# Optimization experiments

Measured on AMD Instinct MI355X. Metric: run time of the kernel, lower is better.

Reference implementation:

```python
import jax, jax.numpy as jnp
import numpy as np

# Regular batched tree: BS roots, arity A, depth D (root=level 0, leaves=level D)
BS, A, D = 32, 4, 6
V, E, H = 50000, 256, 256
LEVEL_SIZES = [BS * A ** d for d in range(D + 1)]
OFFSETS = np.concatenate([[0], np.cumsum(LEVEL_SIZES)]).astype(np.int64)
TOTAL = int(OFFSETS[-1])  # 174752


def gru_cell(x, h, w_ih, w_hh, b_ih, b_hh):
    # torch nn.GRU single step, gate order (r, z, n)
    gi = x @ w_ih.T + b_ih
    gh = h @ w_hh.T + b_hh
    ir, iz, inn = jnp.split(gi, 3, axis=-1)
    hr, hz, hn = jnp.split(gh, 3, axis=-1)
    r = jax.nn.sigmoid(ir + hr)
    z = jax.nn.sigmoid(iz + hz)
    n = jnp.tanh(inn + r * hn)
    return (1.0 - z) * n + z * h


def child_attention(h_last, sent_weight, sent_bias, context_weight):
    # Reproduces hidden_per_child stacking: ch[g,c,i,:] = h_last[g,c] if c==i else 0.
    G, S, _ = h_last.shape
    eye = jnp.eye(S, dtype=h_last.dtype)
    ch = h_last[:, :, None, :] * eye[None, :, :, None]          # [G,S(c),S(i),H]
    t1 = jnp.tanh(jnp.einsum('gcih,hk->gcik', ch, sent_weight) + sent_bias[0])
    u = jnp.tanh(jnp.einsum('gcik,ko->gci', t1, context_weight))  # [G,S,S]
    w = jax.nn.softmax(u, axis=1)                                # softmax over c (the P axis)
    return jnp.einsum('gci,gcih->gih', w, ch)                    # [G,S,H]


def setup_inputs() -> dict:
    key = jax.random.key(0)
    ks = jax.random.split(key, 9)
    s = 1.0 / np.sqrt(H)
    return {
        'tokens': jax.random.randint(ks[0], (TOTAL,), 0, V, dtype=jnp.int32),
        'embedding': jax.random.normal(ks[1], (V, E), jnp.float32) * 0.1,
        'w_ih': jax.random.uniform(ks[2], (3 * H, E), jnp.float32, -s, s),
        'w_hh': jax.random.uniform(ks[3], (3 * H, H), jnp.float32, -s, s),
        'b_ih': jax.random.uniform(ks[4], (3 * H,), jnp.float32, -s, s),
        'b_hh': jax.random.uniform(ks[5], (3 * H,), jnp.float32, -s, s),
        'sent_weight': jax.random.normal(ks[6], (H, H), jnp.float32) * 0.05,
        'sent_bias': jax.random.normal(ks[7], (1, H), jnp.float32) * 0.05,
        'context_weight': jax.random.normal(ks[8], (H, 1), jnp.float32) * 0.05,
    }


def reference(tokens, embedding, w_ih, w_hh, b_ih, b_hh, sent_weight, sent_bias, context_weight):
    def tok(d):
        return tokens[int(OFFSETS[d]):int(OFFSETS[d + 1])]

    gru = lambda x, h: gru_cell(x, h, w_ih, w_hh, b_ih, b_hh)

    # leaves: no children -> zero initial hidden
    h_levels = {D: gru(embedding[tok(D)], jnp.zeros((LEVEL_SIZES[D], H), jnp.float32))}

    for d in range(D - 1, -1, -1):
        h_child = h_levels[d + 1].reshape(-1, A, H)   # [N_d, A, H]
        # duplicate index_copy in torch: only last child's hidden survives per parent
        h_last = h_child[:, A - 1, :]                 # [N_d, H]
        S = BS if d == 0 else A                       # call size: bs at root, A siblings otherwise
        groups = h_last.reshape(-1, S, H)
        chs = child_attention(groups, sent_weight, sent_bias, context_weight).reshape(-1, H)
        h_levels[d] = gru(embedding[tok(d)], chs)

    # final max over node_list: root entry has all bs rows; every other call's entry has
    # only row b = hn of the LAST sibling (duplicate valid_indices), zeros elsewhere.
    out = jnp.maximum(jnp.zeros((BS, H), jnp.float32), h_levels[0])
    for d in range(1, D + 1):
        last_sib = h_levels[d].reshape(BS, -1, A, H)[:, :, A - 1, :].max(axis=1)
        out = jnp.maximum(out, last_sib)
    return out
```

## Files before the change

kernel.cpp:

```cpp
#include <hip/hip_runtime.h>
#include <hip/hip_bf16.h>
#include <math.h>


typedef unsigned short u16;
typedef unsigned int u32;
typedef __attribute__((ext_vector_type(8))) short s8;
typedef __attribute__((ext_vector_type(4))) float f4;
#define MFMA16(a, b, c) __builtin_amdgcn_mfma_f32_16x16x32_bf16(a, b, c, 0, 0, 0)

__device__ __forceinline__ u16 f2bf(float f) {
  u32 x = __float_as_uint(f);
  return (u16)((x + 0x7fffu + ((x >> 16) & 1u)) >> 16);
}
__device__ __forceinline__ float bf2f(u16 u) { return __uint_as_float(((u32)u) << 16); }
__device__ __forceinline__ float sigmoidf_(float x) {
  return __builtin_amdgcn_rcpf(1.f + __builtin_amdgcn_exp2f(-1.4426950408889634f * x));
}
__device__ __forceinline__ float tanhf_(float x) {
  x = fminf(fmaxf(x, -15.f), 15.f);
  float t = __builtin_amdgcn_exp2f(-2.8853900817779268f * x);
  return 1.f - 2.f * t * __builtin_amdgcn_rcpf(1.f + t);
}
__device__ __forceinline__ void gload_lds16(const void* g, void* l) {
  typedef const __attribute__((address_space(1))) unsigned int* gp_t;
  typedef __attribute__((address_space(3))) unsigned int* lp_t;
  __builtin_amdgcn_global_load_lds((gp_t)g, (lp_t)l, 16, 0, 0);
}
__device__ __forceinline__ void stage_row(const float* __restrict__ emb, int tok,
                                          u16* aX, int r, int lane) {
  float4 v = ((const float4*)(emb + (size_t)tok * 256))[lane];
  uint2 val = {(u32)f2bf(v.x) | ((u32)f2bf(v.y) << 16),
               (u32)f2bf(v.z) | ((u32)f2bf(v.w) << 16)};
  *(uint2*)&aX[r * 256 + ((((lane >> 1)) ^ (r & 7)) << 3) + (lane & 1) * 4] = val;
}

__global__ void prep_pack(const float* __restrict__ wih, const float* __restrict__ whh,
                          const float* __restrict__ sw, const float* __restrict__ sb,
                          const float* __restrict__ cw,
                          u16* __restrict__ wihP, u16* __restrict__ whhPh,
                          u16* __restrict__ whhPl, u16* __restrict__ swPh,
                          float* __restrict__ u0p, int* __restrict__ outI) {
  int b = blockIdx.x, t = threadIdx.x;
  if (b == 320) {
    #pragma unroll
    for (int k = 0; k < 32; ++k) outI[k * 256 + t] = 0;
    if (t < 64) {
      float s = 0.f;
      #pragma unroll
      for (int q = 0; q < 4; ++q) { int k = t + 64 * q; s += tanhf(sb[k]) * cw[k]; }
      #pragma unroll
      for (int off = 32; off >= 1; off >>= 1) s += __shfl_xor(s, off);
      if (t == 0) u0p[0] = tanhf(s);
    }
    return;
  }
  int g = b * 256 + t;
  const float* src;
  u16* dst;
  int idx, NF, lomode, trans;
  if (g < 24576)      { idx = g;         src = wih; dst = wihP;  NF = 48; lomode = 0; trans = 1; }
  else if (g < 49152) { idx = g - 24576; src = whh; dst = whhPh; NF = 48; lomode = 0; trans = 1; }
  else if (g < 73728) { idx = g - 49152; src = whh; dst = whhPl; NF = 48; lomode = 1; trans = 1; }
  else                { idx = g - 73728; src = sw;  dst = swPh;  NF = 16; lomode = 0; trans = 0; }
  int lane = idx & 63;
  int t2 = idx >> 6;
  int nf = t2 % NF, kb = t2 / NF;
  int n = nf * 16 + (lane & 15);
  int k0 = kb * 32 + (lane >> 4) * 8;
  float v[8];
  if (trans) {
    const float4* p = (const float4*)(src + (size_t)n * 256 + k0);
    float4 a = p[0], b2 = p[1];
    v[0] = a.x; v[1] = a.y; v[2] = a.z; v[3] = a.w;
    v[4] = b2.x; v[5] = b2.y; v[6] = b2.z; v[7] = b2.w;
  } else {
    #pragma unroll
    for (int j = 0; j < 8; ++j) v[j] = src[(size_t)(k0 + j) * 256 + n];
  }
  u16 o[8];
  #pragma unroll
  for (int j = 0; j < 8; ++j) {
    u16 hi = f2bf(v[j]);
    o[j] = lomode ? f2bf(v[j] - bf2f(hi)) : hi;
  }
  u32* d = (u32*)(dst + (size_t)idx * 8);
  #pragma unroll
  for (int j = 0; j < 4; ++j) d[j] = (u32)o[2 * j] | ((u32)o[2 * j + 1] << 16);
}

__global__ __launch_bounds__(512, 2)
void levelAB_kernel(const int* __restrict__ t6, const int* __restrict__ t5,
                    const float* __restrict__ emb,
                    const u16* __restrict__ wihP, const u16* __restrict__ whhPh,
                    const u16* __restrict__ whhPl, const u16* __restrict__ swPh,
                    const float* __restrict__ bih, const float* __restrict__ bhh,
                    const float* __restrict__ sb, const float* __restrict__ cw,
                    const float* __restrict__ u0p,
                    u16* __restrict__ Hs5Hi, u16* __restrict__ Hs5Lo,
                    int* __restrict__ outI) {
  __shared__ u16 aX6[32768];
  __shared__ u16 aX5[8192];
  __shared__ u16 aH[2][8192];
  __shared__ float pm[8][32];
  __shared__ float scl[32];

  const int t = threadIdx.x;
  const int rb = blockIdx.x;
  const int lane = t & 63, w = t >> 6;
  const int asub = lane >> 4, l15 = lane & 15;
  const float LN3 = 1.0986122886681098f;

  {
    #pragma unroll
    for (int rr = 0; rr < 16; ++rr) {
      int r = 16 * w + rr;
      int tok = t6[4 * (128 * rb + r) + 3];
      stage_row(emb, tok, aX6, r, lane);
    }
    #pragma unroll
    for (int rr = 0; rr < 4; ++rr) {
      int r = 4 * w + rr;
      int tok = t5[4 * (32 * rb + r) + 3];
      stage_row(emb, tok, aX5, r, lane);
    }
  }
  __syncthreads();

  #pragma unroll 1
  for (int pass = 0; pass < 4; ++pass) {
    const int sp = pass >> 1, jc = pass & 1;
    const int cfx = 2 * w + jc;
    f4 gi[3][4];
    #pragma unroll
    for (int g = 0; g < 3; ++g)
      #pragma unroll
      for (int mf = 0; mf < 4; ++mf) gi[g][mf] = (f4){0.f, 0.f, 0.f, 0.f};
    s8 bw[2][3];
    auto LB = [&](int kb, int pb) {
      #pragma unroll
      for (int g = 0; g < 3; ++g)
        bw[pb][g] = *(const s8*)&wihP[((size_t)(kb * 48 + 16 * g + cfx) * 64 + lane) * 8];
    };
    LB(0, 0);
    #pragma unroll
    for (int kb = 0; kb < 8; ++kb) {
      const int pb = kb & 1;
      if (kb < 7) LB(kb + 1, pb ^ 1);
      s8 axh[4];
      #pragma unroll
      for (int mf = 0; mf < 4; ++mf) {
        int abase = (64 * sp + 16 * mf + l15) * 256 + (((kb * 4 + asub) ^ (l15 & 7)) << 3);
        axh[mf] = *(const s8*)&aX6[abase];
      }
      #pragma unroll
      for (int g = 0; g < 3; ++g)
        #pragma unroll
        for (int mf = 0; mf < 4; ++mf)
          gi[g][mf] = MFMA16(axh[mf], bw[pb][g], gi[g][mf]);
    }
    const int col = 16 * cfx + l15;
    const float bi0 = bih[col], bi1 = bih[256 + col], bi2 = bih[512 + col];
    const float bh0 = bhh[col], bh1 = bhh[256 + col], bh2 = bhh[512 + col];
    float cm = -1e30f;
    #pragma unroll
    for (int mf = 0; mf < 4; ++mf) {
      #pragma unroll
      for (int j = 0; j < 4; ++j) {
        float r = sigmoidf_(gi[0][mf][j] + bi0 + bh0);
        float z = sigmoidf_(gi[1][mf][j] + bi1 + bh1);
        float n = tanhf_(gi[2][mf][j] + bi2 + r * bh2);
        float h = (1.f - z) * n;
        if (j == 3) {
          int ci = 16 * sp + 4 * mf + asub;
          u16 hi = f2bf(h);
          u16 lo = f2bf(h - bf2f(hi));
          int hidx = ((col >> 3) * 32 + ci) * 8 + (col & 7);
          aH[0][hidx] = hi;
          aH[1][hidx] = lo;
        }
        cm = fmaxf(cm, h);
      }
    }
    cm = fmaxf(cm, __shfl_xor(cm, 16));
    cm = fmaxf(cm, __shfl_xor(cm, 32));
    if (asub == 0)
      atomicMax(outI + (size_t)(rb >> 3) * 256 + col, __float_as_int(cm));
  }
  __syncthreads();

  f4 sa[2][2];
  #pragma unroll
  for (int jc = 0; jc < 2; ++jc)
    #pragma unroll
    for (int mf = 0; mf < 2; ++mf) sa[jc][mf] = (f4){0.f, 0.f, 0.f, 0.f};
  {
    s8 bsw[2][2];
    auto LSW = [&](int kb, int pb) {
      #pragma unroll
      for (int jc = 0; jc < 2; ++jc)
        bsw[pb][jc] = *(const s8*)&swPh[((size_t)(kb * 16 + 2 * w + jc) * 64 + lane) * 8];
    };
    LSW(0, 0);
    #pragma unroll
    for (int kb = 0; kb < 8; ++kb) {
      const int pb = kb & 1;
      if (kb < 7) LSW(kb + 1, pb ^ 1);
      s8 ahh[2], ahl[2];
      #pragma unroll
      for (int mf = 0; mf < 2; ++mf) {
        int abase = ((kb * 4 + asub) * 32 + 16 * mf + l15) * 8;
        ahh[mf] = *(const s8*)&aH[0][abase];
        ahl[mf] = *(const s8*)&aH[1][abase];
      }
      #pragma unroll
      for (int jc = 0; jc < 2; ++jc) {
        sa[jc][0] = MFMA16(ahh[0], bsw[pb][jc], sa[jc][0]);
        sa[jc][1] = MFMA16(ahh[1], bsw[pb][jc], sa[jc][1]);
        sa[jc][0] = MFMA16(ahl[0], bsw[pb][jc], sa[jc][0]);
        sa[jc][1] = MFMA16(ahl[1], bsw[pb][jc], sa[jc][1]);
      }
    }
  }
  {
    float part[2][4] = {{0.f, 0.f, 0.f, 0.f}, {0.f, 0.f, 0.f, 0.f}};
    #pragma unroll
    for (int jc = 0; jc < 2; ++jc) {
      int k = 16 * (2 * w + jc) + l15;
      float sbk = sb[k], cwk = cw[k];
      #pragma unroll
      for (int mf = 0; mf < 2; ++mf)
        #pragma unroll
        for (int j = 0; j < 4; ++j) part[mf][j] += tanhf_(sa[jc][mf][j] + sbk) * cwk;
    }
    #pragma unroll
    for (int mf = 0; mf < 2; ++mf)
      #pragma unroll
      for (int j = 0; j < 4; ++j) {
        part[mf][j] += __shfl_xor(part[mf][j], 1);
        part[mf][j] += __shfl_xor(part[mf][j], 2);
        part[mf][j] += __shfl_xor(part[mf][j], 4);
        part[mf][j] += __shfl_xor(part[mf][j], 8);
      }
    if (l15 == 0) {
      #pragma unroll
      for (int mf = 0; mf < 2; ++mf)
        #pragma unroll
        for (int j = 0; j < 4; ++j) pm[w][16 * mf + 4 * asub + j] = part[mf][j];
    }
    __syncthreads();
    if (t < 32) {
      float v = 0.f;
      #pragma unroll
      for (int q = 0; q < 8; ++q) v += pm[q][t];
      scl[t] = sigmoidf_(tanhf_(v) - u0p[0] - LN3);
    }
    __syncthreads();
  }
  #pragma unroll 1
  for (int pass = 0; pass < 4; ++pass) {
    const int p = pass >> 1, mf = pass & 1;
    const int cf = w + 8 * p;
    f4 gi5[3], gh5[3];
    #pragma unroll
    for (int g = 0; g < 3; ++g) {
      gi5[g] = (f4){0.f, 0.f, 0.f, 0.f};
      gh5[g] = (f4){0.f, 0.f, 0.f, 0.f};
    }
    #pragma unroll
    for (int kb = 0; kb < 8; ++kb) {
      s8 bwi[3], bwh[3], bwl[3];
      #pragma unroll
      for (int g = 0; g < 3; ++g) {
        size_t bo = ((size_t)(kb * 48 + 16 * g + cf) * 64 + lane) * 8;
        bwi[g] = *(const s8*)&wihP[bo];
        bwh[g] = *(const s8*)&whhPh[bo];
        bwl[g] = *(const s8*)&whhPl[bo];
      }
      int axb = (16 * mf + l15) * 256 + (((kb * 4 + asub) ^ (l15 & 7)) << 3);
      s8 axh = *(const s8*)&aX5[axb];
      int abase = ((kb * 4 + asub) * 32 + 16 * mf + l15) * 8;
      s8 ahh = *(const s8*)&aH[0][abase];
      s8 ahl = *(const s8*)&aH[1][abase];
      #pragma unroll
      for (int g = 0; g < 3; ++g) {
        gi5[g] = MFMA16(axh, bwi[g], gi5[g]);
        gh5[g] = MFMA16(ahh, bwh[g], gh5[g]);
        gh5[g] = MFMA16(ahl, bwh[g], gh5[g]);
        gh5[g] = MFMA16(ahh, bwl[g], gh5[g]);
      }
    }
    const int col = 16 * cf + l15;
    const float bi0 = bih[col], bi1 = bih[256 + col], bi2 = bih[512 + col];
    const float bh0 = bhh[col], bh1 = bhh[256 + col], bh2 = bhh[512 + col];
    const int r0 = 16 * mf + 4 * asub;
    float cm = -1e30f;
    #pragma unroll
    for (int j = 0; j < 4; ++j) {
      const int row = r0 + j;
      const int i = 32 * rb + row;
      float sc = scl[row];
      float ir = gi5[0][j] + bi0;
      float iz = gi5[1][j] + bi1;
      float inn = gi5[2][j] + bi2;
      float g0 = bh0 + sc * gh5[0][j];
      float g1 = bh1 + sc * gh5[1][j];
      float g2 = bh2 + sc * gh5[2][j];
      int hidx = ((col >> 3) * 32 + row) * 8 + (col & 7);
      float hp = sc * (bf2f(aH[0][hidx]) + bf2f(aH[1][hidx]));
      float r = sigmoidf_(ir + g0);
      float z = sigmoidf_(iz + g1);
      float n = tanhf_(inn + r * g2);
      float h = (1.f - z) * n + z * hp;
      if (j == 3) {
        u16 hi = f2bf(h);
        u16 lo = f2bf(h - bf2f(hi));
        Hs5Hi[(size_t)(i >> 2) * 256 + col] = hi;
        Hs5Lo[(size_t)(i >> 2) * 256 + col] = lo;
      }
      cm = fmaxf(cm, h);
    }
    cm = fmaxf(cm, __shfl_xor(cm, 16));
    cm = fmaxf(cm, __shfl_xor(cm, 32));
    if (asub == 0)
      atomicMax(outI + (size_t)(rb >> 3) * 256 + col, __float_as_int(cm));
  }
}

__global__ __launch_bounds__(512, 2)
void levelB_kernel(const int* __restrict__ tokens, const float* __restrict__ emb,
                   const u16* __restrict__ wihP, const u16* __restrict__ whhPh,
                   const u16* __restrict__ whhPl, const u16* __restrict__ swPh,
                   const float* __restrict__ bih, const float* __restrict__ bhh,
                   const float* __restrict__ sb, const float* __restrict__ cw,
                   const float* __restrict__ u0p,
                   const u16* __restrict__ HpHi, const u16* __restrict__ HpLo,
                   u16* __restrict__ HoutHi, u16* __restrict__ HoutLo,
                   int* __restrict__ outI, float logSm1, int bshift) {
  __shared__ u16 aX[8192];
  __shared__ u16 aH[2][8192];
  __shared__ float pm[8][32];
  __shared__ float scl[32];

  const int t = threadIdx.x;
  const int rb = blockIdx.x >> 1, cb = blockIdx.x & 1;
  const int i0 = rb * 32;
  const int lane = t & 63, w = t >> 6;

  {
    int row = lane & 31;
    const u16* sh = HpHi + ((size_t)(i0 + row) << 8);
    const u16* sl = HpLo + ((size_t)(i0 + row) << 8);
    #pragma unroll
    for (int c = 0; c < 2; ++c) {
      int cg = w * 4 + c * 2 + (lane >> 5);
      int lb = w * 1024 + c * 512;
      gload_lds16(sh + (cg << 3), &aH[0][lb]);
      gload_lds16(sl + (cg << 3), &aH[1][lb]);
    }
  }
  {
    #pragma unroll
    for (int rr = 0; rr < 4; ++rr) {
      int r = 4 * w + rr;
      int tok = tokens[4 * (i0 + r) + 3];
      stage_row(emb, tok, aX, r, lane);
    }
  }
  __syncthreads();

  const int asub = lane >> 4, l15 = lane & 15;
  const int cfg = 8 * cb + w;

  f4 gi[3][2], gh[3][2], sa[2][2];
  #pragma unroll
  for (int g = 0; g < 3; ++g)
    #pragma unroll
    for (int mf = 0; mf < 2; ++mf) {
      gi[g][mf] = (f4){0.f, 0.f, 0.f, 0.f};
      gh[g][mf] = (f4){0.f, 0.f, 0.f, 0.f};
    }
  #pragma unroll
  for (int jc = 0; jc < 2; ++jc)
    #pragma unroll
    for (int mf = 0; mf < 2; ++mf) sa[jc][mf] = (f4){0.f, 0.f, 0.f, 0.f};

  #pragma unroll
  for (int kb = 0; kb < 8; ++kb) {
    s8 bwi[3], bwh[3], bwl[3], bsw[2];
    #pragma unroll
    for (int g = 0; g < 3; ++g) {
      size_t bo = ((size_t)(kb * 48 + 16 * g + cfg) * 64 + lane) * 8;
      bwi[g] = *(const s8*)&wihP[bo];
      bwh[g] = *(const s8*)&whhPh[bo];
      bwl[g] = *(const s8*)&whhPl[bo];
    }
    #pragma unroll
    for (int jc = 0; jc < 2; ++jc) {
      size_t so = ((size_t)(kb * 16 + 2 * w + jc) * 64 + lane) * 8;
      bsw[jc] = *(const s8*)&swPh[so];
    }
    s8 axh[2], ahh[2], ahl[2];
    #pragma unroll
    for (int mf = 0; mf < 2; ++mf) {
      int axb = (16 * mf + l15) * 256 + (((kb * 4 + asub) ^ (l15 & 7)) << 3);
      axh[mf] = *(const s8*)&aX[axb];
      int abase = ((kb * 4 + asub) * 32 + 16 * mf + l15) * 8;
      ahh[mf] = *(const s8*)&aH[0][abase];
      ahl[mf] = *(const s8*)&aH[1][abase];
    }
    #pragma unroll
    for (int g = 0; g < 3; ++g) {
      gi[g][0] = MFMA16(axh[0], bwi[g], gi[g][0]);
      gi[g][1] = MFMA16(axh[1], bwi[g], gi[g][1]);
      gh[g][0] = MFMA16(ahh[0], bwh[g], gh[g][0]);
      gh[g][1] = MFMA16(ahh[1], bwh[g], gh[g][1]);
      gh[g][0] = MFMA16(ahl[0], bwh[g], gh[g][0]);
      gh[g][1] = MFMA16(ahl[1], bwh[g], gh[g][1]);
      gh[g][0] = MFMA16(ahh[0], bwl[g], gh[g][0]);
      gh[g][1] = MFMA16(ahh[1], bwl[g], gh[g][1]);
    }
    #pragma unroll
    for (int jc = 0; jc < 2; ++jc) {
      sa[jc][0] = MFMA16(ahh[0], bsw[jc], sa[jc][0]);
      sa[jc][1] = MFMA16(ahh[1], bsw[jc], sa[jc][1]);
      sa[jc][0] = MFMA16(ahl[0], bsw[jc], sa[jc][0]);
      sa[jc][1] = MFMA16(ahl[1], bsw[jc], sa[jc][1]);
    }
  }

  {
    float part[2][4] = {{0.f, 0.f, 0.f, 0.f}, {0.f, 0.f, 0.f, 0.f}};
    #pragma unroll
    for (int jc = 0; jc < 2; ++jc) {
      int k = 16 * (2 * w + jc) + l15;
      float sbk = sb[k], cwk = cw[k];
      #pragma unroll
      for (int mf = 0; mf < 2; ++mf)
        #pragma unroll
        for (int j = 0; j < 4; ++j) part[mf][j] += tanhf_(sa[jc][mf][j] + sbk) * cwk;
    }
    #pragma unroll
    for (int mf = 0; mf < 2; ++mf)
      #pragma unroll
      for (int j = 0; j < 4; ++j) {
        part[mf][j] += __shfl_xor(part[mf][j], 1);
        part[mf][j] += __shfl_xor(part[mf][j], 2);
        part[mf][j] += __shfl_xor(part[mf][j], 4);
        part[mf][j] += __shfl_xor(part[mf][j], 8);
      }
    if (l15 == 0) {
      #pragma unroll
      for (int mf = 0; mf < 2; ++mf)
        #pragma unroll
        for (int j = 0; j < 4; ++j) pm[w][16 * mf + 4 * asub + j] = part[mf][j];
    }
    __syncthreads();
    if (t < 32) {
      float v = 0.f;
      #pragma unroll
      for (int q = 0; q < 8; ++q) v += pm[q][t];
      scl[t] = sigmoidf_(tanhf_(v) - u0p[0] - logSm1);
    }
    __syncthreads();
  }

  {
    const int col = 16 * cfg + l15;
    const float bi0 = bih[col], bi1 = bih[256 + col], bi2 = bih[512 + col];
    const float bh0 = bhh[col], bh1 = bhh[256 + col], bh2 = bhh[512 + col];
    float cmax = -1e30f;
    #pragma unroll
    for (int mf = 0; mf < 2; ++mf) {
      const int r0 = 16 * mf + 4 * asub;
      #pragma unroll
      for (int j = 0; j < 4; ++j) {
        const int row = r0 + j;
        const int i = i0 + row;
        float sc = scl[row];
        float ir = gi[0][mf][j] + bi0;
        float iz = gi[1][mf][j] + bi1;
        float inn = gi[2][mf][j] + bi2;
        float g0 = bh0 + sc * gh[0][mf][j];
        float g1 = bh1 + sc * gh[1][mf][j];
        float g2 = bh2 + sc * gh[2][mf][j];
        int hidx = ((col >> 3) * 32 + row) * 8 + (col & 7);
        float hp = sc * (bf2f(aH[0][hidx]) + bf2f(aH[1][hidx]));
        float r = sigmoidf_(ir + g0);
        float z = sigmoidf_(iz + g1);
        float n = tanhf_(inn + r * g2);
        float h = (1.f - z) * n + z * hp;
        if ((i & 3) == 3) {
          u16 hi = f2bf(h);
          u16 lo = f2bf(h - bf2f(hi));
          HoutHi[(size_t)(i >> 2) * 256 + col] = hi;
          HoutLo[(size_t)(i >> 2) * 256 + col] = lo;
        }
        cmax = fmaxf(cmax, h);
      }
    }
    cmax = fmaxf(cmax, __shfl_xor(cmax, 16));
    cmax = fmaxf(cmax, __shfl_xor(cmax, 32));
    if (asub == 0)
      atomicMax(outI + (size_t)(i0 >> bshift) * 256 + col, __float_as_int(cmax));
  }
}

struct Bregs {
  s8 wi[3], wh[3], wl[3], sw[4];
};
__device__ __forceinline__ void loadB(int kb, int cf, int wq, int lane,
                                      const u16* __restrict__ wihP,
                                      const u16* __restrict__ whhPh,
                                      const u16* __restrict__ whhPl,
                                      const u16* __restrict__ swPh, Bregs& r) {
  #pragma unroll
  for (int g = 0; g < 3; ++g) {
    size_t bo = ((size_t)(kb * 48 + 16 * g + cf) * 64 + lane) * 8;
    r.wi[g] = *(const s8*)&wihP[bo];
    r.wh[g] = *(const s8*)&whhPh[bo];
    r.wl[g] = *(const s8*)&whhPl[bo];
  }
  #pragma unroll
  for (int c = 0; c < 4; ++c) {
    size_t so = ((size_t)(kb * 16 + 4 * wq + c) * 64 + lane) * 8;
    r.sw[c] = *(const s8*)&swPh[so];
  }
}

template <bool ROOT>
__global__ __launch_bounds__(512, 2)
void tail_kernel(const int* __restrict__ tokens, const float* __restrict__ emb,
                 const u16* __restrict__ wihP, const u16* __restrict__ whhPh,
                 const u16* __restrict__ whhPl, const u16* __restrict__ swPh,
                 const float* __restrict__ bih, const float* __restrict__ bhh,
                 const float* __restrict__ sb, const float* __restrict__ cw,
                 const float* __restrict__ u0p,
                 const u16* __restrict__ HpHi, const u16* __restrict__ HpLo,
                 u16* __restrict__ HoutHi, u16* __restrict__ HoutLo,
                 int* __restrict__ outI, float logSm1, int bshift, int store_mode) {
  __shared__ u16 aX[8192];
  __shared__ u16 aH[2][8192];
  __shared__ float pm[8][32];
  __shared__ float scl[32];

  const int t = threadIdx.x;
  const int rb = blockIdx.x >> 2, cb = blockIdx.x & 3;
  const int i0 = rb * 32;
  const int lane = t & 63, w = t >> 6;

  {
    int row = lane & 31;
    const u16* sh = HpHi + ((size_t)(i0 + row) << 8);
    const u16* sl = HpLo + ((size_t)(i0 + row) << 8);
    #pragma unroll
    for (int c = 0; c < 2; ++c) {
      int cg = w * 4 + c * 2 + (lane >> 5);
      int lb = w * 1024 + c * 512;
      gload_lds16(sh + (cg << 3), &aH[0][lb]);
      gload_lds16(sl + (cg << 3), &aH[1][lb]);
    }
  }
  {
    #pragma unroll
    for (int rr = 0; rr < 4; ++rr) {
      int r = 4 * w + rr;
      int tok = tokens[ROOT ? (i0 + r) : (4 * (i0 + r) + 3)];
      stage_row(emb, tok, aX, r, lane);
    }
  }
  __syncthreads();

  const int wq = w & 3, mf = w >> 2;
  const int asub = lane >> 4;
  const int l15 = lane & 15;
  const int cf = 4 * cb + wq;

  f4 gi[3], gh[3], sa[4];
  #pragma unroll
  for (int g = 0; g < 3; ++g) { gi[g] = (f4){0.f, 0.f, 0.f, 0.f}; gh[g] = (f4){0.f, 0.f, 0.f, 0.f}; }
  #pragma unroll
  for (int c = 0; c < 4; ++c) sa[c] = (f4){0.f, 0.f, 0.f, 0.f};

  Bregs b0, b1;
  loadB(0, cf, wq, lane, wihP, whhPh, whhPl, swPh, b0);

  #pragma unroll
  for (int kb = 0; kb < 8; ++kb) {
    Bregs& cur = (kb & 1) ? b1 : b0;
    Bregs& nxt = (kb & 1) ? b0 : b1;
    if (kb < 7) loadB(kb + 1, cf, wq, lane, wihP, whhPh, whhPl, swPh, nxt);
    int axb = (16 * mf + l15) * 256 + (((kb * 4 + asub) ^ (l15 & 7)) << 3);
    s8 axh = *(const s8*)&aX[axb];
    int abase = ((kb * 4 + asub) * 32 + 16 * mf + l15) * 8;
    s8 ahh = *(const s8*)&aH[0][abase];
    s8 ahl = *(const s8*)&aH[1][abase];
    #pragma unroll
    for (int g = 0; g < 3; ++g) {
      gi[g] = MFMA16(axh, cur.wi[g], gi[g]);
      gh[g] = MFMA16(ahh, cur.wh[g], gh[g]);
      gh[g] = MFMA16(ahl, cur.wh[g], gh[g]);
      gh[g] = MFMA16(ahh, cur.wl[g], gh[g]);
    }
    #pragma unroll
    for (int c = 0; c < 4; ++c) {
      sa[c] = MFMA16(ahh, cur.sw[c], sa[c]);
      sa[c] = MFMA16(ahl, cur.sw[c], sa[c]);
    }
  }

  {
    float part[4] = {0.f, 0.f, 0.f, 0.f};
    #pragma unroll
    for (int c = 0; c < 4; ++c) {
      int k = 16 * (4 * wq + c) + l15;
      float sbk = sb[k], cwk = cw[k];
      #pragma unroll
      for (int j = 0; j < 4; ++j) part[j] += tanhf_(sa[c][j] + sbk) * cwk;
    }
    #pragma unroll
    for (int j = 0; j < 4; ++j) {
      part[j] += __shfl_xor(part[j], 1);
      part[j] += __shfl_xor(part[j], 2);
      part[j] += __shfl_xor(part[j], 4);
      part[j] += __shfl_xor(part[j], 8);
    }
    if (l15 == 0) {
      #pragma unroll
      for (int j = 0; j < 4; ++j) pm[w][16 * mf + 4 * asub + j] = part[j];
    }
    __syncthreads();
    if (t < 32) {
      int q0 = (t >> 4) * 4;
      float v = pm[q0][t] + pm[q0 + 1][t] + pm[q0 + 2][t] + pm[q0 + 3][t];
      scl[t] = sigmoidf_(tanhf_(v) - u0p[0] - logSm1);
    }
    __syncthreads();
  }

  {
    const int col = 16 * cf + l15;
    const float bi0 = bih[col], bi1 = bih[256 + col], bi2 = bih[512 + col];
    const float bh0 = bhh[col], bh1 = bhh[256 + col], bh2 = bhh[512 + col];
    const int r0 = 16 * mf + 4 * asub;
    float hmax = -1e30f;
    #pragma unroll
    for (int j = 0; j < 4; ++j) {
      const int row = r0 + j;
      const int i = i0 + row;
      float sc = scl[row];
      float ir = gi[0][j] + bi0;
      float iz = gi[1][j] + bi1;
      float inn = gi[2][j] + bi2;
      float g0 = bh0 + sc * gh[0][j];
      float g1 = bh1 + sc * gh[1][j];
      float g2 = bh2 + sc * gh[2][j];
      int hidx = ((col >> 3) * 32 + row) * 8 + (col & 7);
      float hp = sc * (bf2f(aH[0][hidx]) + bf2f(aH[1][hidx]));
      float r = sigmoidf_(ir + g0);
      float z = sigmoidf_(iz + g1);
      float n = tanhf_(inn + r * g2);
      float h = (1.f - z) * n + z * hp;
      if (store_mode == 1) {
        u16 hi = f2bf(h);
        u16 lo = f2bf(h - bf2f(hi));
        HoutHi[(size_t)i * 256 + col] = hi;
        HoutLo[(size_t)i * 256 + col] = lo;
      } else if (store_mode == 2 && ((i & 3) == 3)) {
        u16 hi = f2bf(h);
        u16 lo = f2bf(h - bf2f(hi));
        HoutHi[(size_t)(i >> 2) * 256 + col] = hi;
        HoutLo[(size_t)(i >> 2) * 256 + col] = lo;
      }
      if (bshift >= 2) {
        hmax = (j == 0) ? h : fmaxf(hmax, h);
      } else {
        atomicMax(outI + (size_t)i * 256 + col, __float_as_int(h));
      }
    }
    if (bshift >= 4) {
      hmax = fmaxf(hmax, __shfl_xor(hmax, 16));
      hmax = fmaxf(hmax, __shfl_xor(hmax, 32));
      if (asub == 0)
        atomicMax(outI + (size_t)((i0 + 16 * mf) >> bshift) * 256 + col,
                  __float_as_int(hmax));
    } else if (bshift >= 2) {
      atomicMax(outI + (size_t)((i0 + r0) >> bshift) * 256 + col, __float_as_int(hmax));
    }
  }
}

extern "C" void kernel_launch(void* const* d_in, const int* in_sizes, int n_in,
                              void* d_out, int out_size, void* d_ws, size_t ws_size,
                              hipStream_t stream) {
  const int*   tokens = (const int*)d_in[0];
  const float* emb    = (const float*)d_in[1];
  const float* wih    = (const float*)d_in[2];
  const float* whh    = (const float*)d_in[3];
  const float* bih    = (const float*)d_in[4];
  const float* bhh    = (const float*)d_in[5];
  const float* sw     = (const float*)d_in[6];
  const float* sb     = (const float*)d_in[7];
  const float* cw     = (const float*)d_in[8];

  char* ws = (char*)d_ws;
  u16* wihP  = (u16*)(ws + 0);
  u16* whhPh = (u16*)(ws + 393216);
  u16* whhPl = (u16*)(ws + 786432);
  u16* swPh  = (u16*)(ws + 1179648);
  float* u0p = (float*)(ws + 1310720);
  u16* H1Hi  = (u16*)(ws + 1310976);
  u16* H1Lo  = (u16*)(ws + 1327360);
  u16* Hs5Hi = (u16*)(ws + 9961472);
  u16* Hs5Lo = (u16*)(ws + 11010048);
  u16* Hs4Hi = (u16*)(ws + 12058624);
  u16* Hs4Lo = (u16*)(ws + 12320768);
  u16* Hs3Hi = (u16*)(ws + 12582912);
  u16* Hs3Lo = (u16*)(ws + 12648448);
  u16* Hs2Hi = (u16*)(ws + 12713984);
  u16* Hs2Lo = (u16*)(ws + 12730368);

  int* outI = (int*)d_out;
  prep_pack<<<321, 256, 0, stream>>>(wih, whh, sw, sb, cw,
                                     wihP, whhPh, whhPl, swPh, u0p, outI);

  const float LN3  = 1.0986122886681098f;
  const float LN31 = 3.4339872044851463f;

  levelAB_kernel<<<256, 512, 0, stream>>>(
      tokens + 43680, tokens + 10912, emb, wihP, whhPh, whhPl, swPh,
      bih, bhh, sb, cw, u0p, Hs5Hi, Hs5Lo, outI);
  levelB_kernel<<<128, 512, 0, stream>>>(
      tokens + 2720, emb, wihP, whhPh, whhPl, swPh, bih, bhh, sb, cw, u0p,
      Hs5Hi, Hs5Lo, Hs4Hi, Hs4Lo, outI, LN3, 6);
  tail_kernel<false><<<64, 512, 0, stream>>>(
      tokens + 672, emb, wihP, whhPh, whhPl, swPh, bih, bhh, sb, cw, u0p,
      Hs4Hi, Hs4Lo, Hs3Hi, Hs3Lo, outI, LN3, 4, 2);
  tail_kernel<false><<<16, 512, 0, stream>>>(
      tokens + 160, emb, wihP, whhPh, whhPl, swPh, bih, bhh, sb, cw, u0p,
      Hs3Hi, Hs3Lo, Hs2Hi, Hs2Lo, outI, LN3, 2, 2);
  tail_kernel<false><<<4, 512, 0, stream>>>(
      tokens + 32, emb, wihP, whhPh, whhPl, swPh, bih, bhh, sb, cw, u0p,
      Hs2Hi, Hs2Lo, H1Hi, H1Lo, outI, LN3, 0, 1);
  tail_kernel<true><<<4, 512, 0, stream>>>(
      tokens + 0, emb, wihP, whhPh, whhPl, swPh, bih, bhh, sb, cw, u0p,
      H1Hi, H1Lo, nullptr, nullptr, outI, LN31, 0, 0);
}
```

Before: 119.9 us.

## Fuse tree levels 3..0 into one per-batch kernel with LDS-resident hidden states

Replaces four tail kernel launches (levels 3, 2, 1 and root) with a single kernel that runs one block per batch tree and carries each level's hidden state through shared memory instead of global round-trips. This removes launch gaps and serialization across tiny grids. In exchange it uses only 32 blocks, so most of each 16-row MFMA tile is padding at levels 1 and 0. It also restructures levelAB's level-5 GRU so both M-fragments share the weight loads, and double-buffers the w_ih loads.

```diff
diff --git a/kernel.cpp b/kernel.cpp
--- a/kernel.cpp
+++ b/kernel.cpp
@@ -110,19 +110,18 @@
   const int lane = t & 63, w = t >> 6;
   const int asub = lane >> 4, l15 = lane & 15;
   const float LN3 = 1.0986122886681098f;
+  const int batch = rb >> 3;
 
   {
     #pragma unroll
     for (int rr = 0; rr < 16; ++rr) {
       int r = 16 * w + rr;
-      int tok = t6[4 * (128 * rb + r) + 3];
-      stage_row(emb, tok, aX6, r, lane);
+      stage_row(emb, t6[4 * (128 * rb + r) + 3], aX6, r, lane);
     }
     #pragma unroll
     for (int rr = 0; rr < 4; ++rr) {
       int r = 4 * w + rr;
-      int tok = t5[4 * (32 * rb + r) + 3];
-      stage_row(emb, tok, aX5, r, lane);
+      stage_row(emb, t5[4 * (32 * rb + r) + 3], aX5, r, lane);
     }
   }
   __syncthreads();
@@ -150,8 +149,8 @@
       s8 axh[4];
       #pragma unroll
       for (int mf = 0; mf < 4; ++mf) {
-        int abase = (64 * sp + 16 * mf + l15) * 256 + (((kb * 4 + asub) ^ (l15 & 7)) << 3);
-        axh[mf] = *(const s8*)&aX6[abase];
+        int ab = (64 * sp + 16 * mf + l15) * 256 + (((kb * 4 + asub) ^ (l15 & 7)) << 3);
+        axh[mf] = *(const s8*)&aX6[ab];
       }
       #pragma unroll
       for (int g = 0; g < 3; ++g)
@@ -185,7 +184,7 @@
     cm = fmaxf(cm, __shfl_xor(cm, 16));
     cm = fmaxf(cm, __shfl_xor(cm, 32));
     if (asub == 0)
-      atomicMax(outI + (size_t)(rb >> 3) * 256 + col, __float_as_int(cm));
+      atomicMax(outI + (size_t)batch * 256 + col, __float_as_int(cm));
   }
   __syncthreads();
 
@@ -209,9 +208,9 @@
       s8 ahh[2], ahl[2];
       #pragma unroll
       for (int mf = 0; mf < 2; ++mf) {
-        int abase = ((kb * 4 + asub) * 32 + 16 * mf + l15) * 8;
-        ahh[mf] = *(const s8*)&aH[0][abase];
-        ahl[mf] = *(const s8*)&aH[1][abase];
+        int ab = ((kb * 4 + asub) * 32 + 16 * mf + l15) * 8;
+        ahh[mf] = *(const s8*)&aH[0][ab];
+        ahl[mf] = *(const s8*)&aH[1][ab];
       }
       #pragma unroll
       for (int jc = 0; jc < 2; ++jc) {
@@ -258,72 +257,106 @@
     __syncthreads();
   }
   #pragma unroll 1
-  for (int pass = 0; pass < 4; ++pass) {
-    const int p = pass >> 1, mf = pass & 1;
+  for (int p = 0; p < 2; ++p) {
     const int cf = w + 8 * p;
-    f4 gi5[3], gh5[3];
-    #pragma unroll
-    for (int g = 0; g < 3; ++g) {
-      gi5[g] = (f4){0.f, 0.f, 0.f, 0.f};
-      gh5[g] = (f4){0.f, 0.f, 0.f, 0.f};
-    }
-    #pragma unroll
-    for (int kb = 0; kb < 8; ++kb) {
-      s8 bwi[3], bwh[3], bwl[3];
-      #pragma unroll
-      for (int g = 0; g < 3; ++g) {
-        size_t bo = ((size_t)(kb * 48 + 16 * g + cf) * 64 + lane) * 8;
-        bwi[g] = *(const s8*)&wihP[bo];
-        bwh[g] = *(const s8*)&whhPh[bo];
-        bwl[g] = *(const s8*)&whhPl[bo];
-      }
-      int axb = (16 * mf + l15) * 256 + (((kb * 4 + asub) ^ (l15 & 7)) << 3);
-      s8 axh = *(const s8*)&aX5[axb];
-      int abase = ((kb * 4 + asub) * 32 + 16 * mf + l15) * 8;
-      s8 ahh = *(const s8*)&aH[0][abase];
-      s8 ahl = *(const s8*)&aH[1][abase];
-      #pragma unroll
-      for (int g = 0; g < 3; ++g) {
-        gi5[g] = MFMA16(axh, bwi[g], gi5[g]);
-        gh5[g] = MFMA16(ahh, bwh[g], gh5[g]);
-        gh5[g] = MFMA16(ahl, bwh[g], gh5[g]);
-        gh5[g] = MFMA16(ahh, bwl[g], gh5[g]);
+    f4 gi5[3][2], gh5[3][2];
+    #pragma unroll
+    for (int g = 0; g < 3; ++g)
+      #pragma unroll
+      for (int mf = 0; mf < 2; ++mf) {
+        gi5[g][mf] = (f4){0.f, 0.f, 0.f, 0.f};
+        gh5[g][mf] = (f4){0.f, 0.f, 0.f, 0.f};
+      }
+    {
+      s8 bwi[2][3];
+      auto LA = [&](int kb, int pb) {
+        #pragma unroll
+        for (int g = 0; g < 3; ++g)
+          bwi[pb][g] = *(const s8*)&wihP[((size_t)(kb * 48 + 16 * g + cf) * 64 + lane) * 8];
+      };
+      LA(0, 0);
+      #pragma unroll
+      for (int kb = 0; kb < 8; ++kb) {
+        const int pb = kb & 1;
+        if (kb < 7) LA(kb + 1, pb ^ 1);
+        s8 axh[2];
+        #pragma unroll
+        for (int mf = 0; mf < 2; ++mf) {
+          int axb = (16 * mf + l15) * 256 + (((kb * 4 + asub) ^ (l15 & 7)) << 3);
+          axh[mf] = *(const s8*)&aX5[axb];
+        }
+        #pragma unroll
+        for (int g = 0; g < 3; ++g) {
+          gi5[g][0] = MFMA16(axh[0], bwi[pb][g], gi5[g][0]);
+          gi5[g][1] = MFMA16(axh[1], bwi[pb][g], gi5[g][1]);
+        }
+      }
+    }
+    {
+      #pragma unroll
+      for (int kb = 0; kb < 8; ++kb) {
+        s8 bwh[3], bwl[3];
+        #pragma unroll
+        for (int g = 0; g < 3; ++g) {
+          size_t bo = ((size_t)(kb * 48 + 16 * g + cf) * 64 + lane) * 8;
+          bwh[g] = *(const s8*)&whhPh[bo];
+          bwl[g] = *(const s8*)&whhPl[bo];
+        }
+        s8 ahh[2], ahl[2];
+        #pragma unroll
+        for (int mf = 0; mf < 2; ++mf) {
+          int ab = ((kb * 4 + asub) * 32 + 16 * mf + l15) * 8;
+          ahh[mf] = *(const s8*)&aH[0][ab];
+          ahl[mf] = *(const s8*)&aH[1][ab];
+        }
+        #pragma unroll
+        for (int g = 0; g < 3; ++g) {
+          gh5[g][0] = MFMA16(ahh[0], bwh[g], gh5[g][0]);
+          gh5[g][1] = MFMA16(ahh[1], bwh[g], gh5[g][1]);
+          gh5[g][0] = MFMA16(ahl[0], bwh[g], gh5[g][0]);
+          gh5[g][1] = MFMA16(ahl[1], bwh[g], gh5[g][1]);
+          gh5[g][0] = MFMA16(ahh[0], bwl[g], gh5[g][0]);
+          gh5[g][1] = MFMA16(ahh[1], bwl[g], gh5[g][1]);
+        }
       }
     }
     const int col = 16 * cf + l15;
     const float bi0 = bih[col], bi1 = bih[256 + col], bi2 = bih[512 + col];
     const float bh0 = bhh[col], bh1 = bhh[256 + col], bh2 = bhh[512 + col];
-    const int r0 = 16 * mf + 4 * asub;
     float cm = -1e30f;
     #pragma unroll
-    for (int j = 0; j < 4; ++j) {
-      const int row = r0 + j;
-      const int i = 32 * rb + row;
-      float sc = scl[row];
-      float ir = gi5[0][j] + bi0;
-      float iz = gi5[1][j] + bi1;
-      float inn = gi5[2][j] + bi2;
-      float g0 = bh0 + sc * gh5[0][j];
-      float g1 = bh1 + sc * gh5[1][j];
-      float g2 = bh2 + sc * gh5[2][j];
-      int hidx = ((col >> 3) * 32 + row) * 8 + (col & 7);
-      float hp = sc * (bf2f(aH[0][hidx]) + bf2f(aH[1][hidx]));
-      float r = sigmoidf_(ir + g0);
-      float z = sigmoidf_(iz + g1);
-      float n = tanhf_(inn + r * g2);
-      float h = (1.f - z) * n + z * hp;
-      if (j == 3) {
-        u16 hi = f2bf(h);
-        u16 lo = f2bf(h - bf2f(hi));
-        Hs5Hi[(size_t)(i >> 2) * 256 + col] = hi;
-        Hs5Lo[(size_t)(i >> 2) * 256 + col] = lo;
-      }
-      cm = fmaxf(cm, h);
+    for (int mf = 0; mf < 2; ++mf) {
+      const int r0 = 16 * mf + 4 * asub;
+      #pragma unroll
+      for (int j = 0; j < 4; ++j) {
+        const int row = r0 + j;
+        const int i = 32 * rb + row;
+        float sc = scl[row];
+        float ir = gi5[0][mf][j] + bi0;
+        float iz = gi5[1][mf][j] + bi1;
+        float inn = gi5[2][mf][j] + bi2;
+        float g0 = bh0 + sc * gh5[0][mf][j];
+        float g1 = bh1 + sc * gh5[1][mf][j];
+        float g2 = bh2 + sc * gh5[2][mf][j];
+        int hidx = ((col >> 3) * 32 + row) * 8 + (col & 7);
+        float hp = sc * (bf2f(aH[0][hidx]) + bf2f(aH[1][hidx]));
+        float r = sigmoidf_(ir + g0);
+        float z = sigmoidf_(iz + g1);
+        float n = tanhf_(inn + r * g2);
+        float h = (1.f - z) * n + z * hp;
+        if (j == 3) {
+          u16 hi = f2bf(h);
+          u16 lo = f2bf(h - bf2f(hi));
+          Hs5Hi[(size_t)(i >> 2) * 256 + col] = hi;
+          Hs5Lo[(size_t)(i >> 2) * 256 + col] = lo;
+        }
+        cm = fmaxf(cm, h);
+      }
     }
     cm = fmaxf(cm, __shfl_xor(cm, 16));
     cm = fmaxf(cm, __shfl_xor(cm, 32));
     if (asub == 0)
-      atomicMax(outI + (size_t)(rb >> 3) * 256 + col, __float_as_int(cm));
+      atomicMax(outI + (size_t)batch * 256 + col, __float_as_int(cm));
   }
 }
 
@@ -506,117 +539,38 @@
   }
 }
 
-struct Bregs {
-  s8 wi[3], wh[3], wl[3], sw[4];
-};
-__device__ __forceinline__ void loadB(int kb, int cf, int wq, int lane,
-                                      const u16* __restrict__ wihP,
-                                      const u16* __restrict__ whhPh,
-                                      const u16* __restrict__ whhPl,
-                                      const u16* __restrict__ swPh, Bregs& r) {
-  #pragma unroll
-  for (int g = 0; g < 3; ++g) {
-    size_t bo = ((size_t)(kb * 48 + 16 * g + cf) * 64 + lane) * 8;
-    r.wi[g] = *(const s8*)&wihP[bo];
-    r.wh[g] = *(const s8*)&whhPh[bo];
-    r.wl[g] = *(const s8*)&whhPl[bo];
-  }
-  #pragma unroll
-  for (int c = 0; c < 4; ++c) {
-    size_t so = ((size_t)(kb * 16 + 4 * wq + c) * 64 + lane) * 8;
-    r.sw[c] = *(const s8*)&swPh[so];
-  }
-}
-
-template <bool ROOT>
-__global__ __launch_bounds__(512, 2)
-void tail_kernel(const int* __restrict__ tokens, const float* __restrict__ emb,
-                 const u16* __restrict__ wihP, const u16* __restrict__ whhPh,
-                 const u16* __restrict__ whhPl, const u16* __restrict__ swPh,
-                 const float* __restrict__ bih, const float* __restrict__ bhh,
-                 const float* __restrict__ sb, const float* __restrict__ cw,
-                 const float* __restrict__ u0p,
-                 const u16* __restrict__ HpHi, const u16* __restrict__ HpLo,
-                 u16* __restrict__ HoutHi, u16* __restrict__ HoutLo,
-                 int* __restrict__ outI, float logSm1, int bshift, int store_mode) {
-  __shared__ u16 aX[8192];
-  __shared__ u16 aH[2][8192];
-  __shared__ float pm[8][32];
-  __shared__ float scl[32];
-
-  const int t = threadIdx.x;
-  const int rb = blockIdx.x >> 2, cb = blockIdx.x & 3;
-  const int i0 = rb * 32;
+__device__ __forceinline__ void level16(
+    const u16* __restrict__ aXp, const u16* __restrict__ aHh,
+    const u16* __restrict__ aHl,
+    const u16* __restrict__ wihP, const u16* __restrict__ whhPh,
+    const u16* __restrict__ whhPl, const u16* __restrict__ swPh,
+    const float* __restrict__ bih, const float* __restrict__ bhh,
+    const float* __restrict__ sb, const float* __restrict__ cw, float u0v,
+    float logSm1, int nvalid, u16* outHh, u16* outHl, int outMode,
+    int* __restrict__ outI, int mode, int batchBase,
+    float (*pm)[32], float* scl, int t) {
   const int lane = t & 63, w = t >> 6;
-
-  {
-    int row = lane & 31;
-    const u16* sh = HpHi + ((size_t)(i0 + row) << 8);
-    const u16* sl = HpLo + ((size_t)(i0 + row) << 8);
-    #pragma unroll
-    for (int c = 0; c < 2; ++c) {
-      int cg = w * 4 + c * 2 + (lane >> 5);
-      int lb = w * 1024 + c * 512;
-      gload_lds16(sh + (cg << 3), &aH[0][lb]);
-      gload_lds16(sl + (cg << 3), &aH[1][lb]);
-    }
-  }
-  {
-    #pragma unroll
-    for (int rr = 0; rr < 4; ++rr) {
-      int r = 4 * w + rr;
-      int tok = tokens[ROOT ? (i0 + r) : (4 * (i0 + r) + 3)];
-      stage_row(emb, tok, aX, r, lane);
-    }
-  }
-  __syncthreads();
-
-  const int wq = w & 3, mf = w >> 2;
-  const int asub = lane >> 4;
-  const int l15 = lane & 15;
-  const int cf = 4 * cb + wq;
-
-  f4 gi[3], gh[3], sa[4];
-  #pragma unroll
-  for (int g = 0; g < 3; ++g) { gi[g] = (f4){0.f, 0.f, 0.f, 0.f}; gh[g] = (f4){0.f, 0.f, 0.f, 0.f}; }
-  #pragma unroll
-  for (int c = 0; c < 4; ++c) sa[c] = (f4){0.f, 0.f, 0.f, 0.f};
-
-  Bregs b0, b1;
-  loadB(0, cf, wq, lane, wihP, whhPh, whhPl, swPh, b0);
-
+  const int asub = lane >> 4, l15 = lane & 15;
+  f4 sa0 = (f4){0.f, 0.f, 0.f, 0.f}, sa1 = (f4){0.f, 0.f, 0.f, 0.f};
   #pragma unroll
   for (int kb = 0; kb < 8; ++kb) {
-    Bregs& cur = (kb & 1) ? b1 : b0;
-    Bregs& nxt = (kb & 1) ? b0 : b1;
-    if (kb < 7) loadB(kb + 1, cf, wq, lane, wihP, whhPh, whhPl, swPh, nxt);
-    int axb = (16 * mf + l15) * 256 + (((kb * 4 + asub) ^ (l15 & 7)) << 3);
-    s8 axh = *(const s8*)&aX[axb];
-    int abase = ((kb * 4 + asub) * 32 + 16 * mf + l15) * 8;
-    s8 ahh = *(const s8*)&aH[0][abase];
-    s8 ahl = *(const s8*)&aH[1][abase];
-    #pragma unroll
-    for (int g = 0; g < 3; ++g) {
-      gi[g] = MFMA16(axh, cur.wi[g], gi[g]);
-      gh[g] = MFMA16(ahh, cur.wh[g], gh[g]);
-      gh[g] = MFMA16(ahl, cur.wh[g], gh[g]);
-      gh[g] = MFMA16(ahh, cur.wl[g], gh[g]);
-    }
-    #pragma unroll
-    for (int c = 0; c < 4; ++c) {
-      sa[c] = MFMA16(ahh, cur.sw[c], sa[c]);
-      sa[c] = MFMA16(ahl, cur.sw[c], sa[c]);
-    }
-  }
-
+    s8 b0 = *(const s8*)&swPh[((size_t)(kb * 16 + 2 * w) * 64 + lane) * 8];
+    s8 b1 = *(const s8*)&swPh[((size_t)(kb * 16 + 2 * w + 1) * 64 + lane) * 8];
+    int ab = ((kb * 4 + asub) * 16 + l15) * 8;
+    s8 ahh = *(const s8*)&aHh[ab];
+    s8 ahl = *(const s8*)&aHl[ab];
+    sa0 = MFMA16(ahh, b0, sa0); sa0 = MFMA16(ahl, b0, sa0);
+    sa1 = MFMA16(ahh, b1, sa1); sa1 = MFMA16(ahl, b1, sa1);
+  }
   {
     float part[4] = {0.f, 0.f, 0.f, 0.f};
     #pragma unroll
-    for (int c = 0; c < 4; ++c) {
-      int k = 16 * (4 * wq + c) + l15;
+    for (int jc = 0; jc < 2; ++jc) {
+      int k = 16 * (2 * w + jc) + l15;
       float sbk = sb[k], cwk = cw[k];
       #pragma unroll
-      for (int j = 0; j < 4; ++j) part[j] += tanhf_(sa[c][j] + sbk) * cwk;
+      for (int j = 0; j < 4; ++j)
+        part[j] += tanhf_((jc ? sa1[j] : sa0[j]) + sbk) * cwk;
     }
     #pragma unroll
     for (int j = 0; j < 4; ++j) {
@@ -627,67 +581,143 @@
     }
     if (l15 == 0) {
       #pragma unroll
-      for (int j = 0; j < 4; ++j) pm[w][16 * mf + 4 * asub + j] = part[j];
+      for (int j = 0; j < 4; ++j) pm[w][4 * asub + j] = part[j];
     }
     __syncthreads();
-    if (t < 32) {
-      int q0 = (t >> 4) * 4;
-      float v = pm[q0][t] + pm[q0 + 1][t] + pm[q0 + 2][t] + pm[q0 + 3][t];
-      scl[t] = sigmoidf_(tanhf_(v) - u0p[0] - logSm1);
+    if (t < 16) {
+      float v = 0.f;
+      #pragma unroll
+      for (int q = 0; q < 8; ++q) v += pm[q][t];
+      scl[t] = sigmoidf_(tanhf_(v) - u0v - logSm1);
     }
     __syncthreads();
   }
-
-  {
+  #pragma unroll 1
+  for (int p = 0; p < 2; ++p) {
+    const int cf = w + 8 * p;
+    f4 gi5[3], gh5[3];
+    #pragma unroll
+    for (int g = 0; g < 3; ++g) {
+      gi5[g] = (f4){0.f, 0.f, 0.f, 0.f};
+      gh5[g] = (f4){0.f, 0.f, 0.f, 0.f};
+    }
+    #pragma unroll
+    for (int kb = 0; kb < 8; ++kb) {
+      s8 bwi[3], bwh[3], bwl[3];
+      #pragma unroll
+      for (int g = 0; g < 3; ++g) {
+        size_t bo = ((size_t)(kb * 48 + 16 * g + cf) * 64 + lane) * 8;
+        bwi[g] = *(const s8*)&wihP[bo];
+        bwh[g] = *(const s8*)&whhPh[bo];
+        bwl[g] = *(const s8*)&whhPl[bo];
+      }
+      int axb = l15 * 256 + (((kb * 4 + asub) ^ (l15 & 7)) << 3);
+      s8 axh = *(const s8*)&aXp[axb];
+      int ab = ((kb * 4 + asub) * 16 + l15) * 8;
+      s8 ahh = *(const s8*)&aHh[ab];
+      s8 ahl = *(const s8*)&aHl[ab];
+      #pragma unroll
+      for (int g = 0; g < 3; ++g) {
+        gi5[g] = MFMA16(axh, bwi[g], gi5[g]);
+        gh5[g] = MFMA16(ahh, bwh[g], gh5[g]);
+        gh5[g] = MFMA16(ahl, bwh[g], gh5[g]);
+        gh5[g] = MFMA16(ahh, bwl[g], gh5[g]);
+      }
+    }
     const int col = 16 * cf + l15;
     const float bi0 = bih[col], bi1 = bih[256 + col], bi2 = bih[512 + col];
     const float bh0 = bhh[col], bh1 = bhh[256 + col], bh2 = bhh[512 + col];
-    const int r0 = 16 * mf + 4 * asub;
-    float hmax = -1e30f;
+    float cm = -1e30f;
     #pragma unroll
     for (int j = 0; j < 4; ++j) {
-      const int row = r0 + j;
-      const int i = i0 + row;
+      const int row = 4 * asub + j;
+      const int valid = row < nvalid;
       float sc = scl[row];
-      float ir = gi[0][j] + bi0;
-      float iz = gi[1][j] + bi1;
-      float inn = gi[2][j] + bi2;
-      float g0 = bh0 + sc * gh[0][j];
-      float g1 = bh1 + sc * gh[1][j];
-      float g2 = bh2 + sc * gh[2][j];
-      int hidx = ((col >> 3) * 32 + row) * 8 + (col & 7);
-      float hp = sc * (bf2f(aH[0][hidx]) + bf2f(aH[1][hidx]));
+      float ir = gi5[0][j] + bi0;
+      float iz = gi5[1][j] + bi1;
+      float inn = gi5[2][j] + bi2;
+      float g0 = bh0 + sc * gh5[0][j];
+      float g1 = bh1 + sc * gh5[1][j];
+      float g2 = bh2 + sc * gh5[2][j];
+      int hix = ((col >> 3) * 16 + row) * 8 + (col & 7);
+      float hp = sc * (bf2f(aHh[hix]) + bf2f(aHl[hix]));
       float r = sigmoidf_(ir + g0);
       float z = sigmoidf_(iz + g1);
       float n = tanhf_(inn + r * g2);
       float h = (1.f - z) * n + z * hp;
-      if (store_mode == 1) {
-        u16 hi = f2bf(h);
-        u16 lo = f2bf(h - bf2f(hi));
-        HoutHi[(size_t)i * 256 + col] = hi;
-        HoutLo[(size_t)i * 256 + col] = lo;
-      } else if (store_mode == 2 && ((i & 3) == 3)) {
-        u16 hi = f2bf(h);
-        u16 lo = f2bf(h - bf2f(hi));
-        HoutHi[(size_t)(i >> 2) * 256 + col] = hi;
-        HoutLo[(size_t)(i >> 2) * 256 + col] = lo;
-      }
-      if (bshift >= 2) {
-        hmax = (j == 0) ? h : fmaxf(hmax, h);
-      } else {
-        atomicMax(outI + (size_t)i * 256 + col, __float_as_int(h));
-      }
-    }
-    if (bshift >= 4) {
-      hmax = fmaxf(hmax, __shfl_xor(hmax, 16));
-      hmax = fmaxf(hmax, __shfl_xor(hmax, 32));
+      u16 hi = f2bf(h);
+      u16 lo = f2bf(h - bf2f(hi));
+      if (outMode == 1 && j == 3 && valid) {
+        int ho = ((col >> 3) * 16 + asub) * 8 + (col & 7);
+        outHh[ho] = hi; outHl[ho] = lo;
+      } else if (outMode == 2 && valid) {
+        outHh[hix] = hi; outHl[hix] = lo;
+      }
+      if (mode == 2) {
+        if (valid)
+          atomicMax(outI + (size_t)(batchBase + row) * 256 + col, __float_as_int(h));
+      } else if (valid) {
+        cm = fmaxf(cm, h);
+      }
+    }
+    if (mode == 0) {
+      cm = fmaxf(cm, __shfl_xor(cm, 16));
+      cm = fmaxf(cm, __shfl_xor(cm, 32));
       if (asub == 0)
-        atomicMax(outI + (size_t)((i0 + 16 * mf) >> bshift) * 256 + col,
-                  __float_as_int(hmax));
-    } else if (bshift >= 2) {
-      atomicMax(outI + (size_t)((i0 + r0) >> bshift) * 256 + col, __float_as_int(hmax));
-    }
-  }
+        atomicMax(outI + (size_t)batchBase * 256 + col, __float_as_int(cm));
+    }
+  }
+}
+
+__global__ __launch_bounds__(512, 2)
+void tailF2_kernel(const int* __restrict__ t3, const int* __restrict__ t2,
+                   const int* __restrict__ t1, const int* __restrict__ t0,
+                   const float* __restrict__ emb,
+                   const u16* __restrict__ wihP, const u16* __restrict__ whhPh,
+                   const u16* __restrict__ whhPl, const u16* __restrict__ swPh,
+                   const float* __restrict__ bih, const float* __restrict__ bhh,
+                   const float* __restrict__ sb, const float* __restrict__ cw,
+                   const float* __restrict__ u0p,
+                   const u16* __restrict__ Hs4Hi, const u16* __restrict__ Hs4Lo,
+                   int* __restrict__ outI) {
+  __shared__ u16 aX3[4096], aH3h[4096], aH3l[4096];
+  __shared__ u16 aX2[4096], aH2h[4096], aH2l[4096];
+  __shared__ u16 aX1[4096], aH1h[4096], aH1l[4096];
+  __shared__ u16 aX0[4096], aH0h[4096], aH0l[4096];
+  __shared__ float pm[8][32];
+  __shared__ float scl[32];
+
+  const int t = threadIdx.x, b = blockIdx.x;
+  const int lane = t & 63, w = t >> 6;
+  const float LN3 = 1.0986122886681098f;
+  const float LN31 = 3.4339872044851463f;
+  const float u0v = u0p[0];
+
+  {
+    int row = t & 15, kg = t >> 4;
+    uint4 vh = *(const uint4*)&Hs4Hi[(size_t)(16 * b + row) * 256 + kg * 8];
+    uint4 vl = *(const uint4*)&Hs4Lo[(size_t)(16 * b + row) * 256 + kg * 8];
+    *(uint4*)&aH3h[(kg * 16 + row) * 8] = vh;
+    *(uint4*)&aH3l[(kg * 16 + row) * 8] = vl;
+    stage_row(emb, t3[4 * (16 * b + w) + 3], aX3, w, lane);
+    stage_row(emb, t3[4 * (16 * b + w + 8) + 3], aX3, w + 8, lane);
+    if (w < 4) stage_row(emb, t2[4 * (4 * b + w) + 3], aX2, w, lane);
+    if (w == 4) stage_row(emb, t1[4 * b + 3], aX1, 0, lane);
+    if (w == 5) stage_row(emb, t0[b], aX0, 0, lane);
+  }
+  __syncthreads();
+
+  level16(aX3, aH3h, aH3l, wihP, whhPh, whhPl, swPh, bih, bhh, sb, cw, u0v,
+          LN3, 16, aH2h, aH2l, 1, outI, 0, b, pm, scl, t);
+  __syncthreads();
+  level16(aX2, aH2h, aH2l, wihP, whhPh, whhPl, swPh, bih, bhh, sb, cw, u0v,
+          LN3, 4, aH1h, aH1l, 1, outI, 0, b, pm, scl, t);
+  __syncthreads();
+  level16(aX1, aH1h, aH1l, wihP, whhPh, whhPl, swPh, bih, bhh, sb, cw, u0v,
+          LN3, 1, aH0h, aH0l, 2, outI, 2, b, pm, scl, t);
+  __syncthreads();
+  level16(aX0, aH0h, aH0l, wihP, whhPh, whhPl, swPh, bih, bhh, sb, cw, u0v,
+          LN31, 1, nullptr, nullptr, 0, outI, 2, b, pm, scl, t);
 }
 
 extern "C" void kernel_launch(void* const* d_in, const int* in_sizes, int n_in,
@@ -709,23 +739,16 @@
   u16* whhPl = (u16*)(ws + 786432);
   u16* swPh  = (u16*)(ws + 1179648);
   float* u0p = (float*)(ws + 1310720);
-  u16* H1Hi  = (u16*)(ws + 1310976);
-  u16* H1Lo  = (u16*)(ws + 1327360);
   u16* Hs5Hi = (u16*)(ws + 9961472);
   u16* Hs5Lo = (u16*)(ws + 11010048);
   u16* Hs4Hi = (u16*)(ws + 12058624);
   u16* Hs4Lo = (u16*)(ws + 12320768);
-  u16* Hs3Hi = (u16*)(ws + 12582912);
-  u16* Hs3Lo = (u16*)(ws + 12648448);
-  u16* Hs2Hi = (u16*)(ws + 12713984);
-  u16* Hs2Lo = (u16*)(ws + 12730368);
 
   int* outI = (int*)d_out;
   prep_pack<<<321, 256, 0, stream>>>(wih, whh, sw, sb, cw,
                                      wihP, whhPh, whhPl, swPh, u0p, outI);
 
-  const float LN3  = 1.0986122886681098f;
-  const float LN31 = 3.4339872044851463f;
+  const float LN3 = 1.0986122886681098f;
 
   levelAB_kernel<<<256, 512, 0, stream>>>(
       tokens + 43680, tokens + 10912, emb, wihP, whhPh, whhPl, swPh,
@@ -733,16 +756,7 @@
   levelB_kernel<<<128, 512, 0, stream>>>(
       tokens + 2720, emb, wihP, whhPh, whhPl, swPh, bih, bhh, sb, cw, u0p,
       Hs5Hi, Hs5Lo, Hs4Hi, Hs4Lo, outI, LN3, 6);
-  tail_kernel<false><<<64, 512, 0, stream>>>(
-      tokens + 672, emb, wihP, whhPh, whhPl, swPh, bih, bhh, sb, cw, u0p,
-      Hs4Hi, Hs4Lo, Hs3Hi, Hs3Lo, outI, LN3, 4, 2);
-  tail_kernel<false><<<16, 512, 0, stream>>>(
-      tokens + 160, emb, wihP, whhPh, whhPl, swPh, bih, bhh, sb, cw, u0p,
-      Hs3Hi, Hs3Lo, Hs2Hi, Hs2Lo, outI, LN3, 2, 2);
-  tail_kernel<false><<<4, 512, 0, stream>>>(
-      tokens + 32, emb, wihP, whhPh, whhPl, swPh, bih, bhh, sb, cw, u0p,
-      Hs2Hi, Hs2Lo, H1Hi, H1Lo, outI, LN3, 0, 1);
-  tail_kernel<true><<<4, 512, 0, stream>>>(
-      tokens + 0, emb, wihP, whhPh, whhPl, swPh, bih, bhh, sb, cw, u0p,
-      H1Hi, H1Lo, nullptr, nullptr, outI, LN31, 0, 0);
-}
+  tailF2_kernel<<<32, 512, 0, stream>>>(
+      tokens + 672, tokens + 160, tokens + 32, tokens, emb,
+      wihP, whhPh, whhPl, swPh, bih, bhh, sb, cw, u0p, Hs4Hi, Hs4Lo, outI);
+}
```

After: 144.9 us. 1.21x slower.
